# Kernel optimization log

Hardware: AMD Instinct MI355X
Metric: run time of the kernel (lower is better)

The kernel has to match this reference:

```python
import jax, jax.numpy as jnp
import numpy as np

B, Q, P, HID = 1, 1024, 1024, 4096
NH, NKV, D = 32, 4, 128
MAXPOS = 2048
N_REP = NH // NKV


def rotate_half(x):
    x1, x2 = jnp.split(x, 2, axis=-1)
    return jnp.concatenate((-x2, x1), axis=-1)


def setup_inputs() -> dict:
    key = jax.random.key(0)
    ks = jax.random.split(key, 8)
    hidden_states = jax.random.normal(ks[0], (B, Q, HID), jnp.float32) * 0.02
    past_key_value = jax.random.normal(ks[1], (B, 2, NKV, P, D), jnp.float32)
    # additive causal mask buffer covering [B, NH, MAXPOS, MAXPOS]
    tril = jnp.tril(jnp.ones((MAXPOS, MAXPOS), jnp.bool_))
    mask2d = jnp.where(tril, 0.0, -1e9).astype(jnp.float32)
    attention_mask = jnp.broadcast_to(mask2d[None, None], (B, NH, MAXPOS, MAXPOS))
    Wq = jax.random.normal(ks[2], (HID, HID), jnp.float32) * 0.02
    Wk = jax.random.normal(ks[3], (NKV * D, HID), jnp.float32) * 0.02
    Wv = jax.random.normal(ks[4], (NKV * D, HID), jnp.float32) * 0.02
    Wo = jax.random.normal(ks[5], (HID, HID), jnp.float32) * 0.02
    return {"hidden_states": hidden_states, "past_key_value": past_key_value,
            "attention_mask": attention_mask, "Wq": Wq, "Wk": Wk, "Wv": Wv, "Wo": Wo}


def reference(hidden_states, past_key_value, attention_mask, Wq, Wk, Wv, Wo):
    kv_len = P + Q
    # projections (torch Linear: y = x @ W^T)
    q = jnp.einsum('bqh,oh->bqo', hidden_states, Wq).reshape(B, Q, NH, D).transpose(0, 2, 1, 3)
    k = jnp.einsum('bqh,oh->bqo', hidden_states, Wk).reshape(B, Q, NKV, D).transpose(0, 2, 1, 3)
    v = jnp.einsum('bqh,oh->bqo', hidden_states, Wv).reshape(B, Q, NKV, D).transpose(0, 2, 1, 3)
    # append to KV cache BEFORE RoPE (faithful to source ordering)
    past_k = past_key_value[:, 0]  # [B, NKV, P, D]
    past_v = past_key_value[:, 1]
    k = jnp.concatenate((past_k, k), axis=2)  # [B, NKV, kv_len, D]
    v = jnp.concatenate((past_v, v), axis=2)
    new_past = jnp.stack((k, v), axis=1)
    # rotary embedding: keys use positions [0, kv_len), queries [P, kv_len)
    inv_freq = 1.0 / (10000.0 ** (jnp.arange(0, D, 2, dtype=jnp.float32) / D))
    t = jnp.arange(kv_len, dtype=jnp.float32)
    freqs = jnp.einsum('i,j->ij', t, inv_freq)
    emb = jnp.concatenate((freqs, freqs), axis=-1)  # [kv_len, D]
    cos = jnp.cos(emb)[None, None]  # [1,1,kv_len,D]
    sin = jnp.sin(emb)[None, None]
    q = q * cos[:, :, P:kv_len] + rotate_half(q) * sin[:, :, P:kv_len]
    k = k * cos + rotate_half(k) * sin
    # causal mask slice: rows [kv_len-Q, kv_len), cols [0, kv_len)
    causal_mask = attention_mask[:, :, P:kv_len, :kv_len]
    # GQA broadcast of KV heads
    k = jnp.repeat(k, N_REP, axis=1)  # [B, NH, kv_len, D]
    v = jnp.repeat(v, N_REP, axis=1)
    scores = jnp.einsum('bhqd,bhkd->bhqk', q, k) / np.sqrt(D).astype(np.float32)
    scores = scores + causal_mask
    probs = jax.nn.softmax(scores, axis=-1)
    ctx = jnp.einsum('bhqk,bhkd->bhqd', probs, v)  # [B, NH, Q, D]
    ctx = ctx.transpose(0, 2, 1, 3).reshape(B, Q, HID)
    attn_output = jnp.einsum('bqh,oh->bqo', ctx, Wo)
    return attn_output, new_past
```

## Files before the change

kernel.cpp:

```cpp
#include <hip/hip_runtime.h>
#include <cstdint>
#include <cstddef>

typedef __attribute__((ext_vector_type(4))) float f32x4;
typedef __attribute__((ext_vector_type(8))) unsigned short u16x8;
typedef __attribute__((ext_vector_type(4))) unsigned short u16x4;
typedef __bf16 bf16x8 __attribute__((ext_vector_type(8)));

__device__ __forceinline__ unsigned short f2bf(float f) {
  unsigned u = __builtin_bit_cast(unsigned, f);
  u += 0x7FFF + ((u >> 16) & 1);
  return (unsigned short)(u >> 16);
}

__device__ __forceinline__ void mfma16x16x32(f32x4& acc, u16x8 a, u16x8 b) {
  acc = __builtin_amdgcn_mfma_f32_16x16x32_bf16(
      __builtin_bit_cast(bf16x8, a), __builtin_bit_cast(bf16x8, b), acc, 0, 0, 0);
}

typedef __attribute__((address_space(1))) const unsigned int as1_u32;
typedef __attribute__((address_space(3))) unsigned int as3_u32;
__device__ __forceinline__ void load_lds16(const void* g, void* l) {
  __builtin_amdgcn_global_load_lds((as1_u32*)g, (as3_u32*)l, 16, 0, 0);
}

#define QSCALE2 0.12751745f

__global__ void k_cvt_small(const float* __restrict__ hs,
                            unsigned short* __restrict__ hs_bf,
                            float2* __restrict__ tab) {
  int i = blockIdx.x * blockDim.x + threadIdx.x;
  if (i < 1048576) {
    float4 v = ((const float4*)hs)[i];
    u16x4 o = { f2bf(v.x), f2bf(v.y), f2bf(v.z), f2bf(v.w) };
    *(u16x4*)(hs_bf + (size_t)i * 4) = o;
  } else {
    int j = i - 1048576;
    int t = j >> 6, f = j & 63;
    float inv = expf(-(float)f * 0.14391156831212787f);
    float ang = (float)t * inv;
    tab[j] = make_float2(cosf(ang), sinf(ang));
  }
}

__global__ __launch_bounds__(256, 3) void k_gemm_bf32(
    const unsigned short* __restrict__ A,
    const float* __restrict__ B1, const float* __restrict__ B2,
    const float* __restrict__ B3, int nb1, int nb2,
    float* __restrict__ C, int M, int N, int K, int KC) {
  __shared__ unsigned short lA[2][128 * 32];
  __shared__ unsigned short lB[2][128 * 32];
  const int tid = threadIdx.x;
  const int w = tid >> 6, lane = tid & 63;
  const int wm = w >> 1, wn = w & 1;
  const int m0 = blockIdx.y * 128, n0 = blockIdx.x * 128;
  const int k0 = blockIdx.z * KC;
  const int lr = lane & 15, lg = lane >> 4;
  float* Cp = C + (size_t)blockIdx.z * M * N;

  const float* bp; int nn;
  if (n0 < nb1)      { bp = B1; nn = n0; }
  else if (n0 < nb2) { bp = B2; nn = n0 - nb1; }
  else               { bp = B3; nn = n0 - nb2; }

  f32x4 acc[4][4];
#pragma unroll
  for (int i = 0; i < 4; i++)
#pragma unroll
    for (int j = 0; j < 4; j++) acc[i][j] = (f32x4){0.f, 0.f, 0.f, 0.f};

  const int srow = w * 32 + (lane >> 2);
  const int scol = (lane & 3) * 8;
  const unsigned short* gA = A + (size_t)(m0 + srow) * K + scol;
  const int br = tid >> 2, bseg = (tid & 3) * 8;
  const float* gB0 = bp + (size_t)(nn + br) * K + bseg;
  const float* gB1 = bp + (size_t)(nn + 64 + br) * K + bseg;

  auto stageA = [&](int buf, int kt) {
#pragma unroll
    for (int c = 0; c < 2; c++)
      load_lds16(gA + (size_t)c * 16 * K + kt, &lA[buf][(w * 32 + c * 16) * 32]);
  };
  auto stageB = [&](int buf, int kt) {
    float4 x0 = *(const float4*)(gB0 + kt);
    float4 x1 = *(const float4*)(gB0 + kt + 4);
    float4 y0 = *(const float4*)(gB1 + kt);
    float4 y1 = *(const float4*)(gB1 + kt + 4);
    u16x8 lo = { f2bf(x0.x), f2bf(x0.y), f2bf(x0.z), f2bf(x0.w),
                 f2bf(x1.x), f2bf(x1.y), f2bf(x1.z), f2bf(x1.w) };
    u16x8 hi = { f2bf(y0.x), f2bf(y0.y), f2bf(y0.z), f2bf(y0.w),
                 f2bf(y1.x), f2bf(y1.y), f2bf(y1.z), f2bf(y1.w) };
    *(u16x8*)&lB[buf][br * 32 + bseg] = lo;
    *(u16x8*)&lB[buf][(64 + br) * 32 + bseg] = hi;
  };

  stageA(0, k0); stageB(0, k0);
  __syncthreads();
  int cur = 0;
  for (int kt = k0; kt < k0 + KC; kt += 32) {
    const bool hasNext = (kt + 32 < k0 + KC);
    if (hasNext) stageA(cur ^ 1, kt + 32);
    u16x8 af[4], bf[4];
#pragma unroll
    for (int i = 0; i < 4; i++) af[i] = *(const u16x8*)&lA[cur][(wm * 64 + i * 16 + lr) * 32 + lg * 8];
#pragma unroll
    for (int j = 0; j < 4; j++) bf[j] = *(const u16x8*)&lB[cur][(wn * 64 + j * 16 + lr) * 32 + lg * 8];
#pragma unroll
    for (int i = 0; i < 4; i++)
#pragma unroll
      for (int j = 0; j < 4; j++) mfma16x16x32(acc[i][j], af[i], bf[j]);
    if (hasNext) stageB(cur ^ 1, kt + 32);
    __syncthreads();
    cur ^= 1;
  }
#pragma unroll
  for (int i = 0; i < 4; i++)
#pragma unroll
    for (int j = 0; j < 4; j++)
#pragma unroll
      for (int r = 0; r < 4; r++) {
        int row = m0 + wm * 64 + i * 16 + lg * 4 + r;
        int col = n0 + wn * 64 + j * 16 + lr;
        Cp[(size_t)row * N + col] = acc[i][j][r];
      }
}

__global__ void k_reduce2(const float4* __restrict__ p, float4* __restrict__ out,
                          int n4, size_t s4) {
  int stridet = gridDim.x * blockDim.x;
  for (int i = blockIdx.x * blockDim.x + threadIdx.x; i < n4; i += stridet) {
    float4 a = p[i], b = p[i + s4];
    out[i] = make_float4(a.x + b.x, a.y + b.y, a.z + b.z, a.w + b.w);
  }
}

#define GP_S 5242880
__device__ __forceinline__ float gsum(const float* __restrict__ gp, size_t i) {
  return gp[i] + gp[i + GP_S];
}

__global__ void k_post(const float* __restrict__ past, const float* __restrict__ gp,
                       float* __restrict__ outk, float* __restrict__ outv,
                       unsigned short* __restrict__ kr, unsigned short* __restrict__ vt,
                       unsigned short* __restrict__ qr, const float2* __restrict__ tab) {
  int idx = blockIdx.x * blockDim.x + threadIdx.x;
  if (idx < 524288) {
    int d0 = idx & 63;
    int t = (idx >> 6) & 2047;
    int h = idx >> 17;
    float v1, v2;
    if (t < 1024) {
      const float* p = past + ((size_t)h * 1024 + t) * 128;
      v1 = p[d0]; v2 = p[d0 + 64];
    } else {
      size_t base = (size_t)(t - 1024) * 5120 + 4096 + h * 128;
      v1 = gsum(gp, base + d0); v2 = gsum(gp, base + d0 + 64);
    }
    float* o = outk + ((size_t)h * 2048 + t) * 128;
    o[d0] = v1; o[d0 + 64] = v2;
    float2 cs = tab[t * 64 + d0];
    unsigned short* ko = kr + ((size_t)h * 2048 + t) * 128;
    ko[d0]      = f2bf(v1 * cs.x - v2 * cs.y);
    ko[d0 + 64] = f2bf(v2 * cs.x + v1 * cs.y);
  } else if (idx < 1572864) {
    int i = idx - 524288;
    int d = i & 127;
    int t = (i >> 7) & 2047;
    int h = i >> 18;
    float val = (t < 1024) ? past[4 * 1024 * 128 + ((size_t)h * 1024 + t) * 128 + d]
                           : gsum(gp, (size_t)(t - 1024) * 5120 + 4608 + h * 128 + d);
    outv[((size_t)h * 2048 + t) * 128 + d] = val;
    vt[((size_t)h * 128 + d) * 2048 + t] = f2bf(val);
  } else {
    int i = idx - 1572864;
    int d0 = i & 63;
    int q = (i >> 6) & 1023;
    int h = i >> 16;
    size_t base = (size_t)q * 5120 + h * 128;
    float v1 = gsum(gp, base + d0), v2 = gsum(gp, base + d0 + 64);
    float2 cs = tab[(1024 + q) * 64 + d0];
    unsigned short* o = qr + ((size_t)h * 1024 + q) * 128;
    o[d0]      = f2bf((v1 * cs.x - v2 * cs.y) * QSCALE2);
    o[d0 + 64] = f2bf((v2 * cs.x + v1 * cs.y) * QSCALE2);
  }
}

__global__ __launch_bounds__(512) void k_attn8(
    const unsigned short* __restrict__ qr,
    const unsigned short* __restrict__ kr,
    const unsigned short* __restrict__ vt,
    unsigned short* __restrict__ ctxb) {
  __shared__ unsigned short k_lds[2][64 * 128];
  __shared__ unsigned short v_lds[2][128 * 64];
  __shared__ unsigned short plds[8][640];
  const int bid = blockIdx.x;
  const int h = bid >> 3;
  const int c = bid & 7;
  const int kvh = h >> 3;
  const int tid = threadIdx.x;
  const int w = tid >> 6, l = tid & 63;
  const int lr = l & 15, lg = l >> 4;
  const int q0 = c * 128 + w * 16;
  const unsigned short* kh = kr + (size_t)kvh * 2048 * 128;
  const unsigned short* vh = vt + (size_t)kvh * 128 * 2048;

  u16x8 qf[4];
  {
    const unsigned short* qb = qr + ((size_t)(h * 1024 + q0 + lr)) * 128 + lg * 8;
#pragma unroll
    for (int ks = 0; ks < 4; ks++) qf[ks] = *(const u16x8*)(qb + ks * 32);
  }
  f32x4 acc[8];
#pragma unroll
  for (int i = 0; i < 8; i++) acc[i] = (f32x4){0.f, 0.f, 0.f, 0.f};
  float m_r = -1e30f, l_r = 0.f;

  const int limit = 1024 + q0 + lr;
  const int mylimit = 1024 + q0 + 15;
  const int T = 18 + 2 * c;

  auto stageK = [&](int buf, int kb) {
#pragma unroll
    for (int i = 0; i < 2; i++) {
      int loff = i * 8192 + tid * 16;
      int row = loff >> 8;
      int scb = (loff & 255) ^ ((row & 7) << 4);
      load_lds16((const char*)(kh + (size_t)(kb + row) * 128) + scb,
                 (char*)&k_lds[buf][0] + loff);
    }
  };
  auto stageV = [&](int buf, int kb) {
#pragma unroll
    for (int i = 0; i < 2; i++) {
      int loff = i * 8192 + tid * 16;
      int row = loff >> 7;
      int scb = (loff & 127) ^ ((row & 7) << 4);
      load_lds16((const char*)(vh + (size_t)row * 2048 + kb) + scb,
                 (char*)&v_lds[buf][0] + loff);
    }
  };

  stageK(0, 0); stageV(0, 0);
  __syncthreads();
  int cur = 0;
  for (int t = 0; t < T; t++) {
    if (t + 1 < T) { stageK(cur ^ 1, (t + 1) * 64); stageV(cur ^ 1, (t + 1) * 64); }
    if (t * 64 <= mylimit) {
#pragma unroll
      for (int kc = 0; kc < 2; kc++) {
        const int kb = t * 64 + kc * 32;
        if (kb > mylimit) continue;
        f32x4 s[2];
#pragma unroll
        for (int sub = 0; sub < 2; sub++) {
          f32x4 a = (f32x4){0.f, 0.f, 0.f, 0.f};
          const int key = kc * 32 + sub * 16 + lr;
          const int swz = (key & 7) << 4;
#pragma unroll
          for (int ks = 0; ks < 4; ks++) {
            int addr = key * 256 + ((ks * 64 + lg * 16) ^ swz);
            u16x8 kf = *(const u16x8*)((const char*)&k_lds[cur][0] + addr);
            mfma16x16x32(a, kf, qf[ks]);
          }
          s[sub] = a;
        }
        float v[8];
#pragma unroll
        for (int r = 0; r < 4; r++) { v[r] = s[0][r]; v[4 + r] = s[1][r]; }
        if (kb + 31 > 1024 + q0) {
          const int kbase = kb + lg * 4;
#pragma unroll
          for (int r = 0; r < 4; r++) {
            if (kbase + r > limit)      v[r]     = -1e30f;
            if (kbase + 16 + r > limit) v[4 + r] = -1e30f;
          }
        }
        float tmax = v[0];
#pragma unroll
        for (int j = 1; j < 8; j++) tmax = fmaxf(tmax, v[j]);
        tmax = fmaxf(tmax, __shfl_xor(tmax, 16));
        tmax = fmaxf(tmax, __shfl_xor(tmax, 32));
        if (!__all(tmax <= m_r + 11.5f)) {
          float mn = fmaxf(m_r, tmax);
          float corr = exp2f(m_r - mn);
          m_r = mn;
          l_r *= corr;
#pragma unroll
          for (int nt = 0; nt < 8; nt++)
#pragma unroll
            for (int r = 0; r < 4; r++) acc[nt][r] *= corr;
        }
        float p[8];
        float psum = 0.f;
#pragma unroll
        for (int j = 0; j < 8; j++) { p[j] = exp2f(v[j] - m_r); psum += p[j]; }
        psum += __shfl_xor(psum, 16);
        psum += __shfl_xor(psum, 32);
        l_r += psum;
        unsigned wds[4];
#pragma unroll
        for (int j = 0; j < 4; j++) {
          unsigned lo = __builtin_bit_cast(unsigned, p[2 * j]) + 0x8000u;
          unsigned hi = __builtin_bit_cast(unsigned, p[2 * j + 1]) + 0x8000u;
          wds[j] = (hi & 0xFFFF0000u) | (lo >> 16);
        }
        char* pb = (char*)&plds[w][0] + lr * 80 + lg * 8;
        *(uint2*)(pb)      = make_uint2(wds[0], wds[1]);
        *(uint2*)(pb + 32) = make_uint2(wds[2], wds[3]);
        asm volatile("s_waitcnt lgkmcnt(0)" ::: "memory");
        u16x8 pf = *(const u16x8*)&plds[w][lr * 40 + lg * 8];
#pragma unroll
        for (int nt = 0; nt < 8; nt++) {
          const int d = nt * 16 + lr;
          int addr = d * 128 + ((kc * 64 + lg * 16) ^ ((d & 7) << 4));
          u16x8 vf = *(const u16x8*)((const char*)&v_lds[cur][0] + addr);
          mfma16x16x32(acc[nt], vf, pf);
        }
      }
    }
    __syncthreads();
    cur ^= 1;
  }
  float inv = 1.0f / l_r;
  unsigned short* ob = ctxb + (size_t)(q0 + lr) * 4096 + h * 128 + lg * 4;
#pragma unroll
  for (int nt = 0; nt < 8; nt++) {
    u16x4 o = { f2bf(acc[nt][0] * inv), f2bf(acc[nt][1] * inv),
                f2bf(acc[nt][2] * inv), f2bf(acc[nt][3] * inv) };
    *(u16x4*)(ob + nt * 16) = o;
  }
}

extern "C" void kernel_launch(void* const* d_in, const int* in_sizes, int n_in,
                              void* d_out, int out_size, void* d_ws, size_t ws_size,
                              hipStream_t stream) {
  (void)in_sizes; (void)n_in; (void)out_size; (void)ws_size;
  const float* hs   = (const float*)d_in[0];
  const float* past = (const float*)d_in[1];
  const float* Wq = (const float*)d_in[3];
  const float* Wk = (const float*)d_in[4];
  const float* Wv = (const float*)d_in[5];
  const float* Wo = (const float*)d_in[6];

  float* out_attn = (float*)d_out;
  float* out_pk = out_attn + 4194304;
  float* out_pv = out_pk + 1048576;

  const size_t MB = 1048576;
  char* ws = (char*)d_ws;
  unsigned short* hs_bf   = (unsigned short*)(ws);
  float2*         tab     = (float2*)(ws + 100 * MB);
  unsigned short* kr      = (unsigned short*)(ws + 101 * MB);
  unsigned short* vt      = (unsigned short*)(ws + 103 * MB);
  unsigned short* qr      = (unsigned short*)(ws + 105 * MB);
  unsigned short* ctxb    = (unsigned short*)(ws + 113 * MB);
  float*          gp      = (float*)(ws + 128 * MB);

  k_cvt_small<<<4608, 256, 0, stream>>>(hs, hs_bf, tab);

  dim3 g1(5120 / 128, 1024 / 128, 2);
  k_gemm_bf32<<<g1, 256, 0, stream>>>(hs_bf, Wq, Wk, Wv, 4096, 4608,
                                      gp, 1024, 5120, 4096, 2048);

  k_post<<<14336, 256, 0, stream>>>(past, gp, out_pk, out_pv, kr, vt, qr, tab);

  k_attn8<<<256, 512, 0, stream>>>(qr, kr, vt, ctxb);

  dim3 g2(4096 / 128, 1024 / 128, 2);
  k_gemm_bf32<<<g2, 256, 0, stream>>>(ctxb, Wo, Wo, Wo, 1 << 30, 1 << 30,
                                      gp, 1024, 4096, 4096, 2048);
  k_reduce2<<<2048, 256, 0, stream>>>((const float4*)gp, (float4*)out_attn,
                                      1048576, 1048576);
}
```

Baseline: 293.6 us.

## Stage fp32 weights via async global-to-LDS loads and raise split-K to four

The B operand (fp32 weights) is now copied straight into LDS as fp32 with global_load_lds and an XOR swizzle. It is converted to bf16 only when fragments are read, which replaces the old register round-trip through f2bf stores. The B prefetch now issues together with A before the MFMAs, so both loads overlap compute. Split-K doubles from 2 to 4 slices, with reductions in k_post and k_reduce4 widened to match. The cost is double the LDS for B (possibly lower occupancy), more partial-sum traffic, and truncation-style bf16 conversion instead of the manual round-to-nearest.

```diff
diff --git a/kernel.cpp b/kernel.cpp
--- a/kernel.cpp
+++ b/kernel.cpp
@@ -49,7 +49,7 @@
     const float* __restrict__ B3, int nb1, int nb2,
     float* __restrict__ C, int M, int N, int K, int KC) {
   __shared__ unsigned short lA[2][128 * 32];
-  __shared__ unsigned short lB[2][128 * 32];
+  __shared__ float lB[2][128 * 32];
   const int tid = threadIdx.x;
   const int w = tid >> 6, lane = tid & 63;
   const int wm = w >> 1, wn = w & 1;
@@ -72,9 +72,6 @@
   const int srow = w * 32 + (lane >> 2);
   const int scol = (lane & 3) * 8;
   const unsigned short* gA = A + (size_t)(m0 + srow) * K + scol;
-  const int br = tid >> 2, bseg = (tid & 3) * 8;
-  const float* gB0 = bp + (size_t)(nn + br) * K + bseg;
-  const float* gB1 = bp + (size_t)(nn + 64 + br) * K + bseg;
 
   auto stageA = [&](int buf, int kt) {
 #pragma unroll
@@ -82,34 +79,45 @@
       load_lds16(gA + (size_t)c * 16 * K + kt, &lA[buf][(w * 32 + c * 16) * 32]);
   };
   auto stageB = [&](int buf, int kt) {
-    float4 x0 = *(const float4*)(gB0 + kt);
-    float4 x1 = *(const float4*)(gB0 + kt + 4);
-    float4 y0 = *(const float4*)(gB1 + kt);
-    float4 y1 = *(const float4*)(gB1 + kt + 4);
-    u16x8 lo = { f2bf(x0.x), f2bf(x0.y), f2bf(x0.z), f2bf(x0.w),
-                 f2bf(x1.x), f2bf(x1.y), f2bf(x1.z), f2bf(x1.w) };
-    u16x8 hi = { f2bf(y0.x), f2bf(y0.y), f2bf(y0.z), f2bf(y0.w),
-                 f2bf(y1.x), f2bf(y1.y), f2bf(y1.z), f2bf(y1.w) };
-    *(u16x8*)&lB[buf][br * 32 + bseg] = lo;
-    *(u16x8*)&lB[buf][(64 + br) * 32 + bseg] = hi;
+#pragma unroll
+    for (int i = 0; i < 4; i++) {
+      int loff = i * 4096 + tid * 16;
+      int row = loff >> 7;
+      int scb = (loff & 127) ^ ((row & 7) << 4);
+      load_lds16((const char*)(bp + (size_t)(nn + row) * K + kt) + scb,
+                 (char*)&lB[buf][0] + loff);
+    }
   };
 
   stageA(0, k0); stageB(0, k0);
   __syncthreads();
   int cur = 0;
   for (int kt = k0; kt < k0 + KC; kt += 32) {
-    const bool hasNext = (kt + 32 < k0 + KC);
-    if (hasNext) stageA(cur ^ 1, kt + 32);
+    if (kt + 32 < k0 + KC) { stageA(cur ^ 1, kt + 32); stageB(cur ^ 1, kt + 32); }
     u16x8 af[4], bf[4];
 #pragma unroll
     for (int i = 0; i < 4; i++) af[i] = *(const u16x8*)&lA[cur][(wm * 64 + i * 16 + lr) * 32 + lg * 8];
 #pragma unroll
-    for (int j = 0; j < 4; j++) bf[j] = *(const u16x8*)&lB[cur][(wn * 64 + j * 16 + lr) * 32 + lg * 8];
+    for (int j = 0; j < 4; j++) {
+      const int row = wn * 64 + j * 16 + lr;
+      const int s = (row & 7) << 4;
+      const char* base = (const char*)&lB[cur][0] + row * 128;
+      f32x4 x = *(const f32x4*)(base + ((lg * 32) ^ s));
+      f32x4 y = *(const f32x4*)(base + ((lg * 32 + 16) ^ s));
+      u16x8 fr = { (unsigned short)__builtin_bit_cast(unsigned short, (__bf16)x[0]),
+                   (unsigned short)__builtin_bit_cast(unsigned short, (__bf16)x[1]),
+                   (unsigned short)__builtin_bit_cast(unsigned short, (__bf16)x[2]),
+                   (unsigned short)__builtin_bit_cast(unsigned short, (__bf16)x[3]),
+                   (unsigned short)__builtin_bit_cast(unsigned short, (__bf16)y[0]),
+                   (unsigned short)__builtin_bit_cast(unsigned short, (__bf16)y[1]),
+                   (unsigned short)__builtin_bit_cast(unsigned short, (__bf16)y[2]),
+                   (unsigned short)__builtin_bit_cast(unsigned short, (__bf16)y[3]) };
+      bf[j] = fr;
+    }
 #pragma unroll
     for (int i = 0; i < 4; i++)
 #pragma unroll
       for (int j = 0; j < 4; j++) mfma16x16x32(acc[i][j], af[i], bf[j]);
-    if (hasNext) stageB(cur ^ 1, kt + 32);
     __syncthreads();
     cur ^= 1;
   }
@@ -125,18 +133,19 @@
       }
 }
 
-__global__ void k_reduce2(const float4* __restrict__ p, float4* __restrict__ out,
-                          int n4, size_t s4) {
+__global__ void k_reduce4(const float4* __restrict__ p, float4* __restrict__ out,
+                          int n4, size_t stride4) {
   int stridet = gridDim.x * blockDim.x;
   for (int i = blockIdx.x * blockDim.x + threadIdx.x; i < n4; i += stridet) {
-    float4 a = p[i], b = p[i + s4];
-    out[i] = make_float4(a.x + b.x, a.y + b.y, a.z + b.z, a.w + b.w);
+    float4 a = p[i], b = p[i + stride4], c = p[i + 2 * stride4], d = p[i + 3 * stride4];
+    out[i] = make_float4((a.x + b.x) + (c.x + d.x), (a.y + b.y) + (c.y + d.y),
+                         (a.z + b.z) + (c.z + d.z), (a.w + b.w) + (c.w + d.w));
   }
 }
 
 #define GP_S 5242880
 __device__ __forceinline__ float gsum(const float* __restrict__ gp, size_t i) {
-  return gp[i] + gp[i + GP_S];
+  return (gp[i] + gp[i + GP_S]) + (gp[i + 2 * (size_t)GP_S] + gp[i + 3 * (size_t)GP_S]);
 }
 
 __global__ void k_post(const float* __restrict__ past, const float* __restrict__ gp,
@@ -358,17 +367,17 @@
 
   k_cvt_small<<<4608, 256, 0, stream>>>(hs, hs_bf, tab);
 
-  dim3 g1(5120 / 128, 1024 / 128, 2);
+  dim3 g1(5120 / 128, 1024 / 128, 4);
   k_gemm_bf32<<<g1, 256, 0, stream>>>(hs_bf, Wq, Wk, Wv, 4096, 4608,
-                                      gp, 1024, 5120, 4096, 2048);
+                                      gp, 1024, 5120, 4096, 1024);
 
   k_post<<<14336, 256, 0, stream>>>(past, gp, out_pk, out_pv, kr, vt, qr, tab);
 
   k_attn8<<<256, 512, 0, stream>>>(qr, kr, vt, ctxb);
 
-  dim3 g2(4096 / 128, 1024 / 128, 2);
+  dim3 g2(4096 / 128, 1024 / 128, 4);
   k_gemm_bf32<<<g2, 256, 0, stream>>>(ctxb, Wo, Wo, Wo, 1 << 30, 1 << 30,
-                                      gp, 1024, 4096, 4096, 2048);
-  k_reduce2<<<2048, 256, 0, stream>>>((const float4*)gp, (float4*)out_attn,
+                                      gp, 1024, 4096, 4096, 1024);
+  k_reduce4<<<2048, 256, 0, stream>>>((const float4*)gp, (float4*)out_attn,
                                       1048576, 1048576);
 }
```

Measured after the change: 299.3 us. No clear change (+2.0%).
